# Kernel optimization log

Measured on AMD Instinct MI355X. Metric: run time of the kernel, lower is better.

The kernel has to match this reference:

```python
import jax, jax.numpy as jnp
import numpy as np

B = 8388608  # batch rows
IN, OUT = 3, 3

def setup_inputs() -> dict:
    key = jax.random.key(0)
    k1, k2, k3 = jax.random.split(key, 3)
    x = jax.random.normal(k1, (B, IN), dtype=jnp.float32) * 5.0  # spread so clamping triggers
    bound = 1.0 / np.sqrt(IN)
    W = jax.random.uniform(k2, (OUT, IN), dtype=jnp.float32, minval=-bound, maxval=bound)
    b = jax.random.uniform(k3, (OUT,), dtype=jnp.float32, minval=-bound, maxval=bound)
    return {"x": x, "W": W, "b": b}

def reference(x, W, b):
    # vectorized physics sim: pos, vel, action = x[:,0], x[:,1], x[:,2]
    vel = x[:, 1] + x[:, 2]
    pos = x[:, 0] + vel
    hit_wall = (pos > 10.0) | (pos < -10.0)
    vel = jnp.where(hit_wall, -vel, vel)
    pos = jnp.clip(pos, -10.0, 10.0)
    reward = -pos * pos
    prediction = jnp.stack([pos, vel, reward], axis=-1)  # [B, 3]
    y = x @ W.T + b  # tiny Linear, [B, 3]
    return prediction + 1e-10 * y
```

## Files before the change

kernel.cpp:

```cpp
#include <hip/hip_runtime.h>


__device__ __forceinline__ void sim_row(float x0, float x1, float x2,
                                        const float* Wv, const float* bv,
                                        float& o0, float& o1, float& o2) {
    float vel = x1 + x2;
    float pos = x0 + vel;
    bool hit = (pos > 10.0f) || (pos < -10.0f);
    vel = hit ? -vel : vel;
    pos = fminf(10.0f, fmaxf(-10.0f, pos));
    float reward = -pos * pos;
    float y0 = fmaf(x0, Wv[0], fmaf(x1, Wv[1], fmaf(x2, Wv[2], bv[0])));
    float y1 = fmaf(x0, Wv[3], fmaf(x1, Wv[4], fmaf(x2, Wv[5], bv[1])));
    float y2 = fmaf(x0, Wv[6], fmaf(x1, Wv[7], fmaf(x2, Wv[8], bv[2])));
    o0 = fmaf(1e-10f, y0, pos);
    o1 = fmaf(1e-10f, y1, vel);
    o2 = fmaf(1e-10f, y2, reward);
}

__global__ __launch_bounds__(256) void HitTheMiddleModel_kernel(
        const float4* __restrict__ X4,
        const float* __restrict__ W,
        const float* __restrict__ B,
        float4* __restrict__ O4,
        const float* __restrict__ X,
        float* __restrict__ O,
        int quads, int rem) {
    int t = blockIdx.x * blockDim.x + threadIdx.x;

    float Wv[9];
#pragma unroll
    for (int i = 0; i < 9; ++i) Wv[i] = W[i];
    float bv[3] = {B[0], B[1], B[2]};

    if (t < quads) {
        const long long base = 3LL * t;
        float4 v0 = X4[base + 0];
        float4 v1 = X4[base + 1];
        float4 v2 = X4[base + 2];
        float4 r0, r1, r2;
        sim_row(v0.x, v0.y, v0.z, Wv, bv, r0.x, r0.y, r0.z);
        sim_row(v0.w, v1.x, v1.y, Wv, bv, r0.w, r1.x, r1.y);
        sim_row(v1.z, v1.w, v2.x, Wv, bv, r1.z, r1.w, r2.x);
        sim_row(v2.y, v2.z, v2.w, Wv, bv, r2.y, r2.z, r2.w);
        O4[base + 0] = r0;
        O4[base + 1] = r1;
        O4[base + 2] = r2;
    } else if (t < quads + rem) {
        long long row = 4LL * quads + (t - quads);
        float x0 = X[3 * row + 0], x1 = X[3 * row + 1], x2 = X[3 * row + 2];
        float o0, o1, o2;
        sim_row(x0, x1, x2, Wv, bv, o0, o1, o2);
        O[3 * row + 0] = o0;
        O[3 * row + 1] = o1;
        O[3 * row + 2] = o2;
    }
}

extern "C" void kernel_launch(void* const* d_in, const int* in_sizes, int n_in,
                              void* d_out, int out_size, void* d_ws, size_t ws_size,
                              hipStream_t stream) {
    const float* x = (const float*)d_in[0];
    const float* W = (const float*)d_in[1];
    const float* b = (const float*)d_in[2];
    float* out = (float*)d_out;

    long long nfloats = (long long)in_sizes[0];
    long long rows = nfloats / 3;
    long long quads = rows / 4;
    int rem = (int)(rows - 4 * quads);

    long long nthreads = quads + rem;
    const int block = 256;
    long long grid = (nthreads + block - 1) / block;

    HitTheMiddleModel_kernel<<<(int)grid, block, 0, stream>>>(
        (const float4*)x, W, b, (float4*)out, x, out, (int)quads, rem);
}
```

Before: 182.7 us.

## Map one thread per output float4 with neighbor-quad halo loads

Changes the work split so each thread produces one output float4 instead of three. Each thread loads its own input float4 plus its left and right neighbors, picks the rows that overlap its output quad by q mod 3, and computes two rows. This gives perfectly coalesced 16-byte stores per lane and triples the thread count, at the cost of three loads per thread (mostly cache hits) and about 1.5x redundant compute.

```diff
diff --git a/kernel.cpp b/kernel.cpp
--- a/kernel.cpp
+++ b/kernel.cpp
@@ -3,7 +3,7 @@
 
 __device__ __forceinline__ void sim_row(float x0, float x1, float x2,
                                         const float* Wv, const float* bv,
-                                        float& o0, float& o1, float& o2) {
+                                        float& pos_o, float& vel_o, float& rew_o) {
     float vel = x1 + x2;
     float pos = x0 + vel;
     bool hit = (pos > 10.0f) || (pos < -10.0f);
@@ -13,9 +13,9 @@
     float y0 = fmaf(x0, Wv[0], fmaf(x1, Wv[1], fmaf(x2, Wv[2], bv[0])));
     float y1 = fmaf(x0, Wv[3], fmaf(x1, Wv[4], fmaf(x2, Wv[5], bv[1])));
     float y2 = fmaf(x0, Wv[6], fmaf(x1, Wv[7], fmaf(x2, Wv[8], bv[2])));
-    o0 = fmaf(1e-10f, y0, pos);
-    o1 = fmaf(1e-10f, y1, vel);
-    o2 = fmaf(1e-10f, y2, reward);
+    pos_o = fmaf(1e-10f, y0, pos);
+    vel_o = fmaf(1e-10f, y1, vel);
+    rew_o = fmaf(1e-10f, y2, reward);
 }
 
 __global__ __launch_bounds__(256) void HitTheMiddleModel_kernel(
@@ -25,35 +25,49 @@
         float4* __restrict__ O4,
         const float* __restrict__ X,
         float* __restrict__ O,
-        int quads, int rem) {
-    int t = blockIdx.x * blockDim.x + threadIdx.x;
+        int n4, int rem) {
+    int q = blockIdx.x * blockDim.x + threadIdx.x;
 
     float Wv[9];
 #pragma unroll
     for (int i = 0; i < 9; ++i) Wv[i] = W[i];
     float bv[3] = {B[0], B[1], B[2]};
 
-    if (t < quads) {
-        const long long base = 3LL * t;
-        float4 v0 = X4[base + 0];
-        float4 v1 = X4[base + 1];
-        float4 v2 = X4[base + 2];
-        float4 r0, r1, r2;
-        sim_row(v0.x, v0.y, v0.z, Wv, bv, r0.x, r0.y, r0.z);
-        sim_row(v0.w, v1.x, v1.y, Wv, bv, r0.w, r1.x, r1.y);
-        sim_row(v1.z, v1.w, v2.x, Wv, bv, r1.z, r1.w, r2.x);
-        sim_row(v2.y, v2.z, v2.w, Wv, bv, r2.y, r2.z, r2.w);
-        O4[base + 0] = r0;
-        O4[base + 1] = r1;
-        O4[base + 2] = r2;
-    } else if (t < quads + rem) {
-        long long row = 4LL * quads + (t - quads);
-        float x0 = X[3 * row + 0], x1 = X[3 * row + 1], x2 = X[3 * row + 2];
-        float o0, o1, o2;
-        sim_row(x0, x1, x2, Wv, bv, o0, o1, o2);
-        O[3 * row + 0] = o0;
-        O[3 * row + 1] = o1;
-        O[3 * row + 2] = o2;
+    if (q < n4) {
+        int iL = (q > 0) ? q - 1 : 0;
+        int iR = (q < n4 - 1) ? q + 1 : q;
+        float4 Lv = X4[iL];
+        float4 Cv = X4[q];
+        float4 Rv = X4[iR];
+        float w0 = Lv.x, w1 = Lv.y, w2 = Lv.z, w3 = Lv.w;
+        float w4 = Cv.x, w5 = Cv.y, w6 = Cv.z, w7 = Cv.w;
+        float w8 = Rv.x, w9 = Rv.y;
+
+        int m = q % 3;
+        float4 r;
+        float pA, vA, rA, pB, vB, rB;
+        if (m == 0) {
+            sim_row(w4, w5, w6, Wv, bv, pA, vA, rA);
+            sim_row(w7, w8, w9, Wv, bv, pB, vB, rB);
+            r = make_float4(pA, vA, rA, pB);
+        } else if (m == 1) {
+            sim_row(w3, w4, w5, Wv, bv, pA, vA, rA);
+            sim_row(w6, w7, w8, Wv, bv, pB, vB, rB);
+            r = make_float4(vA, rA, pB, vB);
+        } else {
+            sim_row(w2, w3, w4, Wv, bv, pA, vA, rA);
+            sim_row(w5, w6, w7, Wv, bv, pB, vB, rB);
+            r = make_float4(rA, pB, vB, rB);
+        }
+        O4[q] = r;
+    } else if (q < n4 + rem) {
+        long long g = 4LL * n4 + (q - n4);
+        long long row = g / 3;
+        int c = (int)(g % 3);
+        float x0 = X[3 * row], x1 = X[3 * row + 1], x2 = X[3 * row + 2];
+        float p, v, rw;
+        sim_row(x0, x1, x2, Wv, bv, p, v, rw);
+        O[g] = (c == 0) ? p : (c == 1) ? v : rw;
     }
 }
 
@@ -66,14 +80,13 @@
     float* out = (float*)d_out;
 
     long long nfloats = (long long)in_sizes[0];
-    long long rows = nfloats / 3;
-    long long quads = rows / 4;
-    int rem = (int)(rows - 4 * quads);
+    long long n4 = nfloats / 4;
+    int rem = (int)(nfloats - 4 * n4);
 
-    long long nthreads = quads + rem;
+    long long nthreads = n4 + rem;
     const int block = 256;
     long long grid = (nthreads + block - 1) / block;
 
     HitTheMiddleModel_kernel<<<(int)grid, block, 0, stream>>>(
-        (const float4*)x, W, b, (float4*)out, x, out, (int)quads, rem);
+        (const float4*)x, W, b, (float4*)out, x, out, (int)n4, rem);
 }
```

Result: faster. 177.4 us (-2.9%).
